# Kernel optimization log

Hardware: AMD Instinct MI355X
Metric: run time of the kernel (lower is better)

## Reference

```python
import jax, jax.numpy as jnp
import numpy as np

B, C, N, K, O = 4, 64, 16384, 16, 128
EPS1, EPS2 = 1e-5, 1e-6


def conv_bn_relu(x, w, g, b, m, v, eps):
    # 1x1 Conv1d (no bias) + eval-mode BatchNorm1d + ReLU; x: [B, C, N]
    y = jnp.einsum('oc,bcn->bon', w, x)
    scale = g / jnp.sqrt(v + eps)
    y = (y - m[None, :, None]) * scale[None, :, None] + b[None, :, None]
    return jax.nn.relu(y)


def gather_neighbors(f_bcn, idx):
    # f_bcn: [B, C, N], idx: [B, N, k] -> [B, C, N, k]
    f_bnc = jnp.transpose(f_bcn, (0, 2, 1))
    g = jax.vmap(lambda f, i: f[i])(f_bnc, idx)  # [B, N, k, C]
    return jnp.transpose(g, (0, 3, 1, 2))


def setup_inputs():
    key = jax.random.key(0)
    ks = jax.random.split(key, 24)
    s = lambda i, shape: jax.random.normal(ks[i], shape, jnp.float32) * 0.05
    inp = {
        'x_info': jax.random.normal(ks[0], (B, C, N, K), jnp.float32),
        'feature': jax.random.normal(ks[1], (B, C, N), jnp.float32),
        'neighbor_index': jax.random.randint(ks[2], (B, N, K), 0, N, jnp.int32),
        'Wq_w': s(3, (C, C)), 'Wq_g': jnp.ones((C,)) + s(4, (C,)), 'Wq_b': s(5, (C,)),
        'Wq_m': s(6, (C,)), 'Wq_v': jax.random.uniform(ks[7], (C,)) + 0.5,
        'Wk_w': s(8, (C, C)), 'Wk_g': jnp.ones((C,)) + s(9, (C,)), 'Wk_b': s(10, (C,)),
        'Wk_m': s(11, (C,)), 'Wk_v': jax.random.uniform(ks[12], (C,)) + 0.5,
        'Wv_w': s(13, (C, C)), 'Wv_g': jnp.ones((C,)) + s(14, (C,)), 'Wv_b': s(15, (C,)),
        'Wv_m': s(16, (C,)), 'Wv_v': jax.random.uniform(ks[17], (C,)) + 0.5,
        'm2_w': s(18, (O, C)), 'm2_g': jnp.ones((O,)) + s(19, (O,)), 'm2_b': s(20, (O,)),
        'm2_m': s(21, (O,)), 'm2_v': jax.random.uniform(ks[22], (O,)) + 0.5,
    }
    return inp


def reference(x_info, feature, neighbor_index,
              Wq_w, Wq_g, Wq_b, Wq_m, Wq_v,
              Wk_w, Wk_g, Wk_b, Wk_m, Wk_v,
              Wv_w, Wv_g, Wv_b, Wv_m, Wv_v,
              m2_w, m2_g, m2_b, m2_m, m2_v):
    q = conv_bn_relu(feature, Wq_w, Wq_g, Wq_b, Wq_m, Wq_v, EPS1)  # [B,C,N]
    k = conv_bn_relu(feature, Wk_w, Wk_g, Wk_b, Wk_m, Wk_v, EPS1)
    v = conv_bn_relu(feature, Wv_w, Wv_g, Wv_b, Wv_m, Wv_v, EPS1)
    kg = gather_neighbors(k, neighbor_index)  # [B,C,N,k]
    vg = gather_neighbors(v, neighbor_index)  # [B,C,N,k]
    W = x_info * (kg - q[..., None])          # [B,C,N,k]
    attn = jax.nn.softmax(W, axis=-1)
    feat = jnp.sum(attn * vg, axis=-1)        # [B,C,N]
    # mlp2: 1x1 conv + BN(eps=1e-6) + LeakyReLU(0.2)
    y = jnp.einsum('oc,bcn->bon', m2_w, feat)
    scale = m2_g / jnp.sqrt(m2_v + EPS2)
    y = (y - m2_m[None, :, None]) * scale[None, :, None] + m2_b[None, :, None]
    return jnp.where(y >= 0, y, 0.2 * y)
```

## Files before the change

kernel.cpp:

```cpp
#include <hip/hip_runtime.h>
#include <cstddef>
#include <cstdint>

#define NPT 16384
#define NB  4

typedef float    f32x4 __attribute__((ext_vector_type(4)));
typedef uint32_t u32x4 __attribute__((ext_vector_type(4)));
typedef uint16_t u16x4 __attribute__((ext_vector_type(4)));

__device__ __forceinline__ uint32_t bf16_rtne(float f) {
    uint32_t u = __builtin_bit_cast(uint32_t, f);
    return (u + 0x7FFFu + ((u >> 16) & 1u)) >> 16;
}
__device__ __forceinline__ float bf16_hi(uint32_t w) {
    return __builtin_bit_cast(float, w & 0xFFFF0000u);
}
__device__ __forceinline__ float bf16_lo(uint32_t w) {
    return __builtin_bit_cast(float, w << 16);
}

__global__ __launch_bounds__(256) void k_qkv(
    const float* __restrict__ feat_in,
    const float* __restrict__ Wq, const float* __restrict__ Wk, const float* __restrict__ Wv,
    const float* __restrict__ Qg, const float* __restrict__ Qb, const float* __restrict__ Qm, const float* __restrict__ Qv,
    const float* __restrict__ Kg, const float* __restrict__ Kb, const float* __restrict__ Km, const float* __restrict__ Kv,
    const float* __restrict__ Vg, const float* __restrict__ Vb, const float* __restrict__ Vm, const float* __restrict__ Vv,
    uint16_t* __restrict__ qo, uint32_t* __restrict__ kvo)
{
    __shared__ float wt[64][192];
    __shared__ float fs[64][64];
    const int tid = threadIdx.x;
    const int b   = blockIdx.y;
    const int n0  = blockIdx.x * 64;

    {
        const int o  = tid >> 2;
        const int cb = (tid & 3) * 16;
        const float* Ws[3] = {Wq, Wk, Wv};
        #pragma unroll
        for (int t = 0; t < 3; ++t) {
            const float4* src = reinterpret_cast<const float4*>(Ws[t] + o * 64 + cb);
            #pragma unroll
            for (int k4 = 0; k4 < 4; ++k4) {
                float4 w4 = src[k4];
                wt[cb + k4 * 4 + 0][t * 64 + o] = w4.x;
                wt[cb + k4 * 4 + 1][t * 64 + o] = w4.y;
                wt[cb + k4 * 4 + 2][t * 64 + o] = w4.z;
                wt[cb + k4 * 4 + 3][t * 64 + o] = w4.w;
            }
        }
    }
    #pragma unroll
    for (int i = 0; i < 16; ++i) {
        int flat = tid + i * 256;
        int c = flat >> 6, n = flat & 63;
        fs[c][n] = feat_in[((size_t)b * 64 + c) * NPT + n0 + n];
    }
    __syncthreads();

    const int to = tid & 15;
    const int tn = tid >> 4;
    float acc[3][4][4];
    #pragma unroll
    for (int t = 0; t < 3; ++t)
        #pragma unroll
        for (int i = 0; i < 4; ++i)
            #pragma unroll
            for (int j = 0; j < 4; ++j) acc[t][i][j] = 0.f;

    #pragma unroll 4
    for (int c = 0; c < 64; ++c) {
        float4 f4  = *reinterpret_cast<const float4*>(&fs[c][tn * 4]);
        float4 wq4 = *reinterpret_cast<const float4*>(&wt[c][to * 4]);
        float4 wk4 = *reinterpret_cast<const float4*>(&wt[c][64 + to * 4]);
        float4 wv4 = *reinterpret_cast<const float4*>(&wt[c][128 + to * 4]);
        float fr[4]    = {f4.x, f4.y, f4.z, f4.w};
        float wr[3][4] = {{wq4.x, wq4.y, wq4.z, wq4.w},
                          {wk4.x, wk4.y, wk4.z, wk4.w},
                          {wv4.x, wv4.y, wv4.z, wv4.w}};
        #pragma unroll
        for (int t = 0; t < 3; ++t)
            #pragma unroll
            for (int oi = 0; oi < 4; ++oi)
                #pragma unroll
                for (int nn = 0; nn < 4; ++nn)
                    acc[t][oi][nn] = fmaf(wr[t][oi], fr[nn], acc[t][oi][nn]);
    }

    float scq[4], shq[4], sck[4], shk[4], scv[4], shv[4];
    #pragma unroll
    for (int oi = 0; oi < 4; ++oi) {
        int o = to * 4 + oi;
        float s;
        s = Qg[o] * rsqrtf(Qv[o] + 1e-5f); scq[oi] = s; shq[oi] = Qb[o] - Qm[o] * s;
        s = Kg[o] * rsqrtf(Kv[o] + 1e-5f); sck[oi] = s; shk[oi] = Kb[o] - Km[o] * s;
        s = Vg[o] * rsqrtf(Vv[o] + 1e-5f); scv[oi] = s; shv[oi] = Vb[o] - Vm[o] * s;
    }
    #pragma unroll
    for (int nn = 0; nn < 4; ++nn) {
        const size_t pidx = (size_t)b * NPT + n0 + tn * 4 + nn;
        u16x4 rq;
        u32x4 pk;
        #pragma unroll
        for (int oi = 0; oi < 4; ++oi) {
            float q = fmaxf(fmaf(acc[0][oi][nn], scq[oi], shq[oi]), 0.f);
            float rk = fmaxf(fmaf(acc[1][oi][nn], sck[oi], shk[oi]), 0.f);
            float rv = fmaxf(fmaf(acc[2][oi][nn], scv[oi], shv[oi]), 0.f);
            rq[oi] = (uint16_t)bf16_rtne(q);
            pk[oi] = (bf16_rtne(rk) << 16) | bf16_rtne(rv);
        }
        *reinterpret_cast<u16x4*>(qo  + (pidx << 6) + to * 4) = rq;
        *reinterpret_cast<u32x4*>(kvo + (pidx << 6) + to * 4) = pk;
    }
}

__global__ __launch_bounds__(256) void k_attn(
    const float*    __restrict__ xinfo,
    const int*      __restrict__ nidx,
    uint16_t*                    qfeat,
    const uint32_t* __restrict__ kv)
{
    __shared__ float xs[64][68];
    const int tid  = threadIdx.x;
    const int lane = tid & 63;
    const int wv   = tid >> 6;
    const int p0   = blockIdx.x * 4;
    const int b    = p0 >> 14;
    const int n0   = p0 & 16383;
    const int p    = p0 + wv;

    const int pu = __builtin_amdgcn_readfirstlane(p);
    const int4* irow = reinterpret_cast<const int4*>(nidx + ((size_t)pu << 4));
    int4 i0 = irow[0], i1 = irow[1], i2 = irow[2], i3 = irow[3];
    const int idxs[16] = {i0.x, i0.y, i0.z, i0.w,  i1.x, i1.y, i1.z, i1.w,
                          i2.x, i2.y, i2.z, i2.w,  i3.x, i3.y, i3.z, i3.w};

    uint32_t gr[16];
    #pragma unroll
    for (int j = 0; j < 16; ++j)
        gr[j] = kv[(((size_t)((b << 14) | idxs[j])) << 6) + lane];

    uint16_t qraw = __builtin_nontemporal_load(qfeat + ((size_t)p << 6) + lane);
    float qc = bf16_lo((uint32_t)qraw);

    const float* xbase = xinfo + (((size_t)b * 64) * NPT + n0) * 16;
    f32x4 xr[4];
    #pragma unroll
    for (int i = 0; i < 4; ++i) {
        int f = tid + i * 256;
        int c = f >> 4, s = f & 15;
        xr[i] = __builtin_nontemporal_load(
            reinterpret_cast<const f32x4*>(xbase + (size_t)c * (NPT * 16) + s * 4));
    }
    #pragma unroll
    for (int i = 0; i < 4; ++i) {
        int f = tid + i * 256;
        int c = f >> 4, s = f & 15;
        *reinterpret_cast<f32x4*>(&xs[c][s * 4]) = xr[i];
    }
    __syncthreads();

    float es = 0.f, fsum = 0.f;
    #pragma unroll
    for (int k4 = 0; k4 < 4; ++k4) {
        float4 x4 = *reinterpret_cast<const float4*>(&xs[lane][wv * 16 + k4 * 4]);
        float xv[4] = {x4.x, x4.y, x4.z, x4.w};
        #pragma unroll
        for (int q4 = 0; q4 < 4; ++q4) {
            int j = k4 * 4 + q4;
            float e = __expf(xv[q4] * (bf16_hi(gr[j]) - qc));
            es += e;
            fsum = fmaf(e, bf16_lo(gr[j]), fsum);
        }
    }

    qfeat[((size_t)p << 6) + lane] = (uint16_t)bf16_rtne(fsum / es);
}

__global__ __launch_bounds__(256) void k_mlp2(
    const uint16_t* __restrict__ feat,
    const float* __restrict__ m2w,
    const float* __restrict__ g2, const float* __restrict__ b2,
    const float* __restrict__ m2, const float* __restrict__ v2,
    float* __restrict__ out)
{
    __shared__ float wt [64][132];
    __shared__ float fsh[64][69];
    const int tid = threadIdx.x;
    const int b   = blockIdx.y;
    const int n0  = blockIdx.x * 64;

    {
        const int o  = tid >> 1;
        const int ch = (tid & 1) * 32;
        const float4* src = reinterpret_cast<const float4*>(m2w + o * 64 + ch);
        #pragma unroll
        for (int k4 = 0; k4 < 8; ++k4) {
            float4 w4 = src[k4];
            wt[ch + k4 * 4 + 0][o] = w4.x;
            wt[ch + k4 * 4 + 1][o] = w4.y;
            wt[ch + k4 * 4 + 2][o] = w4.z;
            wt[ch + k4 * 4 + 3][o] = w4.w;
        }
    }
    {
        const int c8 = tid & 7;
        const int nl = tid >> 3;
        #pragma unroll
        for (int half = 0; half < 2; ++half) {
            int n = nl + half * 32;
            u32x4 rw = *reinterpret_cast<const u32x4*>(
                feat + (((size_t)b * NPT + n0 + n) << 6) + c8 * 8);
            #pragma unroll
            for (int k = 0; k < 4; ++k) {
                uint32_t w2 = rw[k];
                fsh[c8 * 8 + k * 2 + 0][n] = bf16_lo(w2);
                fsh[c8 * 8 + k * 2 + 1][n] = bf16_hi(w2);
            }
        }
    }
    __syncthreads();

    const int tn = tid & 15;
    const int to = tid >> 4;
    float acc[2][4][4];
    #pragma unroll
    for (int h = 0; h < 2; ++h)
        #pragma unroll
        for (int i = 0; i < 4; ++i)
            #pragma unroll
            for (int j = 0; j < 4; ++j) acc[h][i][j] = 0.f;

    #pragma unroll 4
    for (int c = 0; c < 64; ++c) {
        float4 wa = *reinterpret_cast<const float4*>(&wt[c][to * 4]);
        float4 wb = *reinterpret_cast<const float4*>(&wt[c][64 + to * 4]);
        float4 f4 = *reinterpret_cast<const float4*>(&fsh[c][tn * 4]);
        float wra[4] = {wa.x, wa.y, wa.z, wa.w};
        float wrb[4] = {wb.x, wb.y, wb.z, wb.w};
        float fr[4]  = {f4.x, f4.y, f4.z, f4.w};
        #pragma unroll
        for (int oi = 0; oi < 4; ++oi)
            #pragma unroll
            for (int ni = 0; ni < 4; ++ni) {
                acc[0][oi][ni] = fmaf(wra[oi], fr[ni], acc[0][oi][ni]);
                acc[1][oi][ni] = fmaf(wrb[oi], fr[ni], acc[1][oi][ni]);
            }
    }

    #pragma unroll
    for (int h = 0; h < 2; ++h)
        #pragma unroll
        for (int oi = 0; oi < 4; ++oi) {
            int o = h * 64 + to * 4 + oi;
            float s  = g2[o] * rsqrtf(v2[o] + 1e-6f);
            float sh = b2[o] - m2[o] * s;
            f32x4 r;
            #pragma unroll
            for (int ni = 0; ni < 4; ++ni) {
                float y = fmaf(acc[h][oi][ni], s, sh);
                r[ni] = (y >= 0.f) ? y : 0.2f * y;
            }
            __builtin_nontemporal_store(r, reinterpret_cast<f32x4*>(
                out + (((size_t)b << 7) + o) * NPT + n0 + tn * 4));
        }
}

extern "C" void kernel_launch(void* const* d_in, const int* in_sizes, int n_in,
                              void* d_out, int out_size, void* d_ws, size_t ws_size,
                              hipStream_t stream)
{
    const float* xinfo   = (const float*)d_in[0];
    const float* feature = (const float*)d_in[1];
    const int*   nidx    = (const int*)  d_in[2];
    const float* Wq = (const float*)d_in[3];
    const float* Qg = (const float*)d_in[4];
    const float* Qb = (const float*)d_in[5];
    const float* Qm = (const float*)d_in[6];
    const float* Qv = (const float*)d_in[7];
    const float* Wk = (const float*)d_in[8];
    const float* Kg = (const float*)d_in[9];
    const float* Kb = (const float*)d_in[10];
    const float* Km = (const float*)d_in[11];
    const float* Kv = (const float*)d_in[12];
    const float* Wv = (const float*)d_in[13];
    const float* Vg = (const float*)d_in[14];
    const float* Vb = (const float*)d_in[15];
    const float* Vm = (const float*)d_in[16];
    const float* Vv = (const float*)d_in[17];
    const float* m2w = (const float*)d_in[18];
    const float* g2  = (const float*)d_in[19];
    const float* b2  = (const float*)d_in[20];
    const float* m2  = (const float*)d_in[21];
    const float* v2  = (const float*)d_in[22];
    float* out = (float*)d_out;

    uint16_t* qf    = (uint16_t*)d_ws;
    uint32_t* kvbuf = (uint32_t*)((uint8_t*)d_ws + (8u << 20));

    k_qkv<<<dim3(NPT / 64, NB), 256, 0, stream>>>(
        feature, Wq, Wk, Wv,
        Qg, Qb, Qm, Qv, Kg, Kb, Km, Kv, Vg, Vb, Vm, Vv,
        qf, kvbuf);

    k_attn<<<(NB * NPT) / 4, 256, 0, stream>>>(xinfo, nidx, qf, kvbuf);

    k_mlp2<<<dim3(NPT / 64, NB), 256, 0, stream>>>(qf, m2w, g2, b2, m2, v2, out);
}
```

Measured before the change: 110.7 us.

## Make attention kernel persistent over four tiles with double-buffered prefetch

The attention kernel now handles four point-tiles per block, a quarter of the former grid size. While it computes the current tile it prefetches the next tile's x_info, neighbour indices, gathered K/V and q into registers. A double-buffered LDS array and explicit barriers hand tiles between iterations, which is meant to hide global-load latency behind the softmax math. In exchange, register pressure and LDS use per block go up and fewer blocks are launched, which may lower occupancy and the latency hiding it provides.

```diff
diff --git a/kernel.cpp b/kernel.cpp
--- a/kernel.cpp
+++ b/kernel.cpp
@@ -4,6 +4,9 @@
 
 #define NPT 16384
 #define NB  4
+
+#define T_TILES  4
+#define GRID_ATT ((NB * NPT / 4) / T_TILES)
 
 typedef float    f32x4 __attribute__((ext_vector_type(4)));
 typedef uint32_t u32x4 __attribute__((ext_vector_type(4)));
@@ -104,7 +107,7 @@
         u32x4 pk;
         #pragma unroll
         for (int oi = 0; oi < 4; ++oi) {
-            float q = fmaxf(fmaf(acc[0][oi][nn], scq[oi], shq[oi]), 0.f);
+            float q  = fmaxf(fmaf(acc[0][oi][nn], scq[oi], shq[oi]), 0.f);
             float rk = fmaxf(fmaf(acc[1][oi][nn], sck[oi], shk[oi]), 0.f);
             float rv = fmaxf(fmaf(acc[2][oi][nn], scv[oi], shv[oi]), 0.f);
             rq[oi] = (uint16_t)bf16_rtne(q);
@@ -121,61 +124,107 @@
     uint16_t*                    qfeat,
     const uint32_t* __restrict__ kv)
 {
-    __shared__ float xs[64][68];
+    __shared__ float xs[2][64][68];
     const int tid  = threadIdx.x;
     const int lane = tid & 63;
     const int wv   = tid >> 6;
-    const int p0   = blockIdx.x * 4;
-    const int b    = p0 >> 14;
-    const int n0   = p0 & 16383;
-    const int p    = p0 + wv;
-
-    const int pu = __builtin_amdgcn_readfirstlane(p);
-    const int4* irow = reinterpret_cast<const int4*>(nidx + ((size_t)pu << 4));
-    int4 i0 = irow[0], i1 = irow[1], i2 = irow[2], i3 = irow[3];
-    const int idxs[16] = {i0.x, i0.y, i0.z, i0.w,  i1.x, i1.y, i1.z, i1.w,
-                          i2.x, i2.y, i2.z, i2.w,  i3.x, i3.y, i3.z, i3.w};
 
     uint32_t gr[16];
-    #pragma unroll
-    for (int j = 0; j < 16; ++j)
-        gr[j] = kv[(((size_t)((b << 14) | idxs[j])) << 6) + lane];
-
-    uint16_t qraw = __builtin_nontemporal_load(qfeat + ((size_t)p << 6) + lane);
-    float qc = bf16_lo((uint32_t)qraw);
-
-    const float* xbase = xinfo + (((size_t)b * 64) * NPT + n0) * 16;
-    f32x4 xr[4];
-    #pragma unroll
-    for (int i = 0; i < 4; ++i) {
-        int f = tid + i * 256;
-        int c = f >> 4, s = f & 15;
-        xr[i] = __builtin_nontemporal_load(
-            reinterpret_cast<const f32x4*>(xbase + (size_t)c * (NPT * 16) + s * 4));
-    }
-    #pragma unroll
-    for (int i = 0; i < 4; ++i) {
-        int f = tid + i * 256;
-        int c = f >> 4, s = f & 15;
-        *reinterpret_cast<f32x4*>(&xs[c][s * 4]) = xr[i];
-    }
-    __syncthreads();
-
-    float es = 0.f, fsum = 0.f;
-    #pragma unroll
-    for (int k4 = 0; k4 < 4; ++k4) {
-        float4 x4 = *reinterpret_cast<const float4*>(&xs[lane][wv * 16 + k4 * 4]);
-        float xv[4] = {x4.x, x4.y, x4.z, x4.w};
-        #pragma unroll
-        for (int q4 = 0; q4 < 4; ++q4) {
-            int j = k4 * 4 + q4;
-            float e = __expf(xv[q4] * (bf16_hi(gr[j]) - qc));
-            es += e;
-            fsum = fmaf(e, bf16_lo(gr[j]), fsum);
-        }
-    }
-
-    qfeat[((size_t)p << 6) + lane] = (uint16_t)bf16_rtne(fsum / es);
+    float    qc;
+    f32x4    xr[4];
+
+    {
+        const int p0 = blockIdx.x * 4;
+        const int b = p0 >> 14, n0 = p0 & 16383, p = p0 + wv;
+        const float* xbase = xinfo + (((size_t)b * 64) * NPT + n0) * 16;
+        #pragma unroll
+        for (int i = 0; i < 4; ++i) {
+            int f = tid + i * 256, c = f >> 4, s = f & 15;
+            xr[i] = __builtin_nontemporal_load(
+                reinterpret_cast<const f32x4*>(xbase + (size_t)c * (NPT * 16) + s * 4));
+        }
+        const int pu = __builtin_amdgcn_readfirstlane(p);
+        const int4* ir = reinterpret_cast<const int4*>(nidx + ((size_t)pu << 4));
+        int4 a0 = ir[0], a1 = ir[1], a2 = ir[2], a3 = ir[3];
+        const int idxs[16] = {a0.x,a0.y,a0.z,a0.w, a1.x,a1.y,a1.z,a1.w,
+                              a2.x,a2.y,a2.z,a2.w, a3.x,a3.y,a3.z,a3.w};
+        #pragma unroll
+        for (int j = 0; j < 16; ++j)
+            gr[j] = kv[(((size_t)((b << 14) | idxs[j])) << 6) + lane];
+        qc = bf16_lo((uint32_t)__builtin_nontemporal_load(
+                 qfeat + ((size_t)p << 6) + lane));
+        #pragma unroll
+        for (int i = 0; i < 4; ++i) {
+            int f = tid + i * 256, c = f >> 4, s = f & 15;
+            *reinterpret_cast<f32x4*>(&xs[0][c][s * 4]) = xr[i];
+        }
+    }
+    asm volatile("s_waitcnt lgkmcnt(0)" ::: "memory");
+    __builtin_amdgcn_sched_barrier(0);
+    __builtin_amdgcn_s_barrier();
+    __builtin_amdgcn_sched_barrier(0);
+
+    #pragma unroll
+    for (int t = 0; t < T_TILES; ++t) {
+        const int cur = t & 1;
+        uint32_t grn[16];
+        float    qn = 0.f;
+
+        if (t + 1 < T_TILES) {
+            const int p0 = (blockIdx.x + (t + 1) * GRID_ATT) * 4;
+            const int b = p0 >> 14, n0 = p0 & 16383, p = p0 + wv;
+            const float* xbase = xinfo + (((size_t)b * 64) * NPT + n0) * 16;
+            #pragma unroll
+            for (int i = 0; i < 4; ++i) {
+                int f = tid + i * 256, c = f >> 4, s = f & 15;
+                xr[i] = __builtin_nontemporal_load(
+                    reinterpret_cast<const f32x4*>(xbase + (size_t)c * (NPT * 16) + s * 4));
+            }
+            const int pu = __builtin_amdgcn_readfirstlane(p);
+            const int4* ir = reinterpret_cast<const int4*>(nidx + ((size_t)pu << 4));
+            int4 a0 = ir[0], a1 = ir[1], a2 = ir[2], a3 = ir[3];
+            const int idxs[16] = {a0.x,a0.y,a0.z,a0.w, a1.x,a1.y,a1.z,a1.w,
+                                  a2.x,a2.y,a2.z,a2.w, a3.x,a3.y,a3.z,a3.w};
+            #pragma unroll
+            for (int j = 0; j < 16; ++j)
+                grn[j] = kv[(((size_t)((b << 14) | idxs[j])) << 6) + lane];
+            qn = bf16_lo((uint32_t)__builtin_nontemporal_load(
+                     qfeat + ((size_t)p << 6) + lane));
+        }
+
+        {
+            const int p = (blockIdx.x + t * GRID_ATT) * 4 + wv;
+            float es = 0.f, fsum = 0.f;
+            #pragma unroll
+            for (int k4 = 0; k4 < 4; ++k4) {
+                float4 x4 = *reinterpret_cast<const float4*>(&xs[cur][lane][wv * 16 + k4 * 4]);
+                float xv[4] = {x4.x, x4.y, x4.z, x4.w};
+                #pragma unroll
+                for (int q4 = 0; q4 < 4; ++q4) {
+                    int j = k4 * 4 + q4;
+                    float e = __expf(xv[q4] * (bf16_hi(gr[j]) - qc));
+                    es += e;
+                    fsum = fmaf(e, bf16_lo(gr[j]), fsum);
+                }
+            }
+            qfeat[((size_t)p << 6) + lane] = (uint16_t)bf16_rtne(fsum / es);
+        }
+
+        if (t + 1 < T_TILES) {
+            #pragma unroll
+            for (int i = 0; i < 4; ++i) {
+                int f = tid + i * 256, c = f >> 4, s = f & 15;
+                *reinterpret_cast<f32x4*>(&xs[cur ^ 1][c][s * 4]) = xr[i];
+            }
+            #pragma unroll
+            for (int j = 0; j < 16; ++j) gr[j] = grn[j];
+            qc = qn;
+            asm volatile("s_waitcnt lgkmcnt(0)" ::: "memory");
+            __builtin_amdgcn_sched_barrier(0);
+            __builtin_amdgcn_s_barrier();
+            __builtin_amdgcn_sched_barrier(0);
+        }
+    }
 }
 
 __global__ __launch_bounds__(256) void k_mlp2(
@@ -304,7 +353,7 @@
         Qg, Qb, Qm, Qv, Kg, Kb, Km, Kv, Vg, Vb, Vm, Vv,
         qf, kvbuf);
 
-    k_attn<<<(NB * NPT) / 4, 256, 0, stream>>>(xinfo, nidx, qf, kvbuf);
+    k_attn<<<GRID_ATT, 256, 0, stream>>>(xinfo, nidx, qf, kvbuf);
 
     k_mlp2<<<dim3(NPT / 64, NB), 256, 0, stream>>>(qf, m2w, g2, b2, m2, v2, out);
 }
```

Result: slower. 121.4 us (+9.6%).
